# Performance work log

Measured on AMD Instinct MI355X. Metric: run time of the kernel, lower is better.

Reference implementation:

```python
import jax, jax.numpy as jnp
import numpy as np

N = 50000   # total nodes
E = 100000  # total edges
F = 64      # input node features
H = 128     # hidden_dim
HEADS = 4
B = 64      # number of graphs in the batch
S = 512     # num_stations
LC = 8      # num_line_colors


def setup_inputs() -> dict:
    key = jax.random.key(0)
    ks = jax.random.split(key, 40)
    w = lambda i, shape: (jax.random.normal(ks[i], shape, jnp.float32) * 0.02)
    inp = {
        'node_features': jax.random.normal(ks[0], (N, F), jnp.float32),
        'edge_index': jax.random.randint(ks[1], (2, E), 0, N),
        'batch': jnp.sort(jax.random.randint(ks[2], (N,), 0, B)),
        # initial projection F -> H
        'Wp': w(3, (F, H)), 'bp': w(4, (H,)),
        # TransformerConv 1: in H, out H, heads HEADS (concat)
        'Wq1': w(5, (H, HEADS * H)), 'bq1': w(6, (HEADS * H,)),
        'Wk1': w(7, (H, HEADS * H)), 'bk1': w(8, (HEADS * H,)),
        'Wv1': w(9, (H, HEADS * H)), 'bv1': w(10, (HEADS * H,)),
        'Ws1': w(11, (H, HEADS * H)), 'bs1': w(12, (HEADS * H,)),
        # TransformerConv 2: in HEADS*H, out H, heads 1
        'Wq2': w(13, (HEADS * H, H)), 'bq2': w(14, (H,)),
        'Wk2': w(15, (HEADS * H, H)), 'bk2': w(16, (H,)),
        'Wv2': w(17, (HEADS * H, H)), 'bv2': w(18, (H,)),
        'Ws2': w(19, (HEADS * H, H)), 'bs2': w(20, (H,)),
        # output heads
        'crW': w(21, (H, 1)),  'crb': w(22, (1,)),
        'hlW': w(23, (H, 4)),  'hlb': w(24, (4,)),
        'mtW': w(25, (H, 3)),  'mtb': w(26, (3,)),
        'p1W': w(27, (H, S)),  'p1b': w(28, (S,)),
        'p2W': w(29, (H, S)),  'p2b': w(30, (S,)),
        'dtW': w(31, (H, S)),  'dtb': w(32, (S,)),
        'slW': w(33, (H, LC)), 'slb': w(34, (LC,)),
    }
    return inp


def transformer_conv(x, src, dst, Wq, bq, Wk, bk, Wv, bv, Ws, bs, heads, out_ch):
    # PyG TransformerConv (beta=False, concat=True, root_weight=True):
    #   alpha_ij = softmax_j( (W_q x_i) . (W_k x_j) / sqrt(d) ) over in-edges of i
    #   out_i    = sum_j alpha_ij * (W_v x_j)  (concat heads) + W_skip x_i
    n = x.shape[0]
    q = (x @ Wq + bq).reshape(n, heads, out_ch)
    k = (x @ Wk + bk).reshape(n, heads, out_ch)
    v = (x @ Wv + bv).reshape(n, heads, out_ch)
    scores = jnp.sum(q[dst] * k[src], axis=-1) / jnp.sqrt(jnp.float32(out_ch))  # [E,heads]
    m = jax.ops.segment_max(scores, dst, num_segments=n)                        # per-target max
    e = jnp.exp(scores - m[dst])
    denom = jax.ops.segment_sum(e, dst, num_segments=n)
    alpha = e / (denom[dst] + 1e-16)                                            # [E,heads]
    out = jax.ops.segment_sum(alpha[:, :, None] * v[src], dst, num_segments=n)  # [N,heads,out]
    return out.reshape(n, heads * out_ch) + (x @ Ws + bs)


def reference(node_features, edge_index, batch, Wp, bp,
              Wq1, bq1, Wk1, bk1, Wv1, bv1, Ws1, bs1,
              Wq2, bq2, Wk2, bk2, Wv2, bv2, Ws2, bs2,
              crW, crb, hlW, hlb, mtW, mtb, p1W, p1b, p2W, p2b, dtW, dtb, slW, slb):
    src, dst = edge_index[0], edge_index[1]
    h = jax.nn.relu(node_features @ Wp + bp)
    h = jax.nn.relu(transformer_conv(h, src, dst, Wq1, bq1, Wk1, bk1, Wv1, bv1, Ws1, bs1, HEADS, H))
    h = jax.nn.relu(transformer_conv(h, src, dst, Wq2, bq2, Wk2, bk2, Wv2, bv2, Ws2, bs2, 1, H))
    # global mean pool over graphs
    counts = jax.ops.segment_sum(jnp.ones((h.shape[0],), h.dtype), batch, num_segments=B)
    g = jax.ops.segment_sum(h, batch, num_segments=B) / jnp.maximum(counts, 1.0)[:, None]  # [B,H]
    value = g @ crW + crb
    return (value,
            g @ hlW + hlb,
            g @ mtW + mtb,
            g @ p1W + p1b,
            g @ p2W + p2b,
            g @ dtW + dtb,
            g @ slW + slb)
```

## Files before the change

kernel.cpp:

```cpp
#include <hip/hip_runtime.h>
#include <hip/hip_bf16.h>

#define NN 50000
#define EE 100000
#define FF 64
#define HH 128
#define HEADS 4
#define BB 64
#define SS 512
#define LCC 8

__device__ __forceinline__ float b2f(ushort u) {
    return __uint_as_float(((unsigned)u) << 16);
}
__device__ __forceinline__ ushort f2b(float f) {
    unsigned u = __float_as_uint(f);
    unsigned r = (u + 0x7FFFu + ((u >> 16) & 1u)) >> 16;
    return (ushort)r;
}
__device__ __forceinline__ uint f2b_pk(float a, float b) {
    __hip_bfloat162 h = __float22bfloat162_rn(make_float2(a, b));
    return *reinterpret_cast<uint*>(&h);
}

__device__ __forceinline__ uint f2fp8x4(float a, float b, float c, float d) {
    int r = __builtin_amdgcn_cvt_pk_fp8_f32(a, b, 0, false);
    r = __builtin_amdgcn_cvt_pk_fp8_f32(c, d, r, true);
    return (uint)r;
}
__device__ __forceinline__ void fp8x4(uint u, float* f) {
    auto lo = __builtin_amdgcn_cvt_pk_f32_fp8((int)u, false);
    auto hi = __builtin_amdgcn_cvt_pk_f32_fp8((int)u, true);
    f[0] = lo[0]; f[1] = lo[1]; f[2] = hi[0]; f[3] = hi[1];
}

typedef __attribute__((ext_vector_type(4))) float f32x4;
typedef __attribute__((ext_vector_type(8))) short s16x8;
typedef __attribute__((ext_vector_type(4))) uint u32x4;

__device__ __forceinline__ void glls16(const ushort* g, ushort* l) {
    __builtin_amdgcn_global_load_lds((const __attribute__((address_space(1))) void*)g,
                                     (__attribute__((address_space(3))) void*)l, 16, 0, 0);
}

#define BM 128
#define BN 128
#define BK 64
#define EST 68

__global__ __launch_bounds__(256) void gemm_bf16(
    const ushort* __restrict__ A, const ushort* __restrict__ Bt,
    const float* __restrict__ bias,
    ushort* __restrict__ C1, int ld1,
    ushort* __restrict__ C2b, int mode,
    int M, int K, int relu, int gx, int gy)
{
    __shared__ __align__(16) ushort Sm[2 * BM * BK];
    ushort* As = Sm;
    ushort* Bs = Sm + BM * BK;

    const int bid  = blockIdx.x;
    const int xcd  = bid & 7;
    const int slot = bid >> 3;
    const int bx   = slot % gx;
    const int by   = xcd + 8 * (slot / gx);
    if (by >= gy) return;
    const int m0 = by * BM;
    const int n0 = bx * BN;

    const int t = threadIdx.x;
    const int lane = t & 63;
    const int wave = t >> 6;
    const int wm = (wave & 1) * 64;
    const int wn = (wave >> 1) * 64;
    const int lrow = lane & 15;
    const int g    = lane >> 4;

    const int wbase = n0 + wn;
    float bj[4];
#pragma unroll
    for (int j = 0; j < 4; ++j) bj[j] = bias[wbase + j * 16 + lrow];

    const int srow = (wave << 5) + (lane >> 3);
    const int scs  = lane & 7;

    const ushort* ga[4];
    const ushort* gb[4];
#pragma unroll
    for (int p = 0; p < 4; ++p) {
        const int row = srow + (p << 3);
        const int l   = scs ^ (row & 7);
        ga[p] = A + (size_t)min(m0 + row, M - 1) * K + (l << 3);
        gb[p] = Bt + (size_t)(n0 + row) * K + (l << 3);
    }
    const int ldsoff = (wave << 11);

    f32x4 acc[4][4];
#pragma unroll
    for (int i = 0; i < 4; ++i)
#pragma unroll
        for (int j = 0; j < 4; ++j)
            acc[i][j] = (f32x4){bj[j], bj[j], bj[j], bj[j]};

    for (int k0 = 0; k0 < K; k0 += BK) {
#pragma unroll
        for (int p = 0; p < 4; ++p) glls16(ga[p] + k0, As + ldsoff + (p << 9));
#pragma unroll
        for (int p = 0; p < 4; ++p) glls16(gb[p] + k0, Bs + ldsoff + (p << 9));
        __syncthreads();

#pragma unroll
        for (int kk = 0; kk < 2; ++kk) {
            s16x8 af[4], bf[4];
#pragma unroll
            for (int i = 0; i < 4; ++i) {
                const int R = wm + i * 16 + lrow;
                const int c = ((kk << 2) + g) ^ (R & 7);
                af[i] = *(const s16x8*)&As[(R << 6) + (c << 3)];
            }
#pragma unroll
            for (int j = 0; j < 4; ++j) {
                const int R = wn + j * 16 + lrow;
                const int c = ((kk << 2) + g) ^ (R & 7);
                bf[j] = *(const s16x8*)&Bs[(R << 6) + (c << 3)];
            }
#pragma unroll
            for (int i = 0; i < 4; ++i)
#pragma unroll
                for (int j = 0; j < 4; ++j)
                    acc[i][j] = __builtin_amdgcn_mfma_f32_16x16x32_bf16(af[i], bf[j], acc[i][j], 0, 0, 0);
        }
        __syncthreads();
    }

    float* Es = (float*)Sm + wave * (16 * EST);

    bool e8 = false;
    ushort* Cw = C1; int ldw = ld1; int cb = wbase;
    unsigned char* Cw8 = nullptr;
    if (mode == 1) {
        e8 = true;
        if (wbase < 512) {
            Cw8 = (unsigned char*)C1;
            ldw = 512;
        } else {
            const int u = wbase - 512;
            const int h = u >> 8;
            cb = u & 255;
            Cw8 = (unsigned char*)C2b + (size_t)h * NN * 256;
            ldw = 256;
        }
    } else if (mode == 2) {
        if (wbase < 128) { ldw = 128; }
        else {
            e8 = true;
            Cw8 = (unsigned char*)C2b;
            ldw = 384;
            cb = wbase - 128;
        }
    }

    const int rbase = (lane >> 4) * 4;
    const int rrow  = lane >> 2;
    const int rcol  = (lane & 3) << 4;

#pragma unroll
    for (int i = 0; i < 4; ++i) {
#pragma unroll
        for (int j = 0; j < 4; ++j)
#pragma unroll
            for (int r = 0; r < 4; ++r) {
                float v = acc[i][j][r];
                if (relu) v = fmaxf(v, 0.f);
                Es[(rbase + r) * EST + j * 16 + lrow] = v;
            }
        const int gm = m0 + wm + i * 16 + rrow;
        if (gm < M) {
            const float* srcp = Es + rrow * EST + rcol;
            f32x4 f0 = *(const f32x4*)(srcp + 0);
            f32x4 f1 = *(const f32x4*)(srcp + 4);
            f32x4 f2 = *(const f32x4*)(srcp + 8);
            f32x4 f3 = *(const f32x4*)(srcp + 12);
            if (!e8) {
                u32x4 o0, o1;
                o0[0] = f2b_pk(f0[0], f0[1]); o0[1] = f2b_pk(f0[2], f0[3]);
                o0[2] = f2b_pk(f1[0], f1[1]); o0[3] = f2b_pk(f1[2], f1[3]);
                o1[0] = f2b_pk(f2[0], f2[1]); o1[1] = f2b_pk(f2[2], f2[3]);
                o1[2] = f2b_pk(f3[0], f3[1]); o1[3] = f2b_pk(f3[2], f3[3]);
                ushort* dst = Cw + (size_t)gm * ldw + cb + rcol;
                *(u32x4*)(dst + 0) = o0;
                *(u32x4*)(dst + 8) = o1;
            } else {
                u32x4 o;
                o[0] = f2fp8x4(f0[0], f0[1], f0[2], f0[3]);
                o[1] = f2fp8x4(f1[0], f1[1], f1[2], f1[3]);
                o[2] = f2fp8x4(f2[0], f2[1], f2[2], f2[3]);
                o[3] = f2fp8x4(f3[0], f3[1], f3[2], f3[3]);
                *(u32x4*)(Cw8 + (size_t)gm * ldw + cb + rcol) = o;
            }
        }
    }
}

#define F1OFF  8192
#define F2OFF  204800
#define WTOTAL 466944
#define BTOT   2048
#define MWORK  (HEADS * 128 * 128 + HEADS * 128)

__global__ void prep_kernel(
    const float* __restrict__ Wp,
    const float* __restrict__ Wq1, const float* __restrict__ Wk1,
    const float* __restrict__ Wv1, const float* __restrict__ Ws1,
    const float* __restrict__ Wq2, const float* __restrict__ Wk2,
    const float* __restrict__ Wv2, const float* __restrict__ Ws2,
    const float* __restrict__ bs1, const float* __restrict__ bq1,
    const float* __restrict__ bv1, const float* __restrict__ bs2,
    const float* __restrict__ bq2, const float* __restrict__ bk2, const float* __restrict__ bv2,
    ushort* __restrict__ wt, float* __restrict__ bb)
{
    int t = blockIdx.x * 256 + threadIdx.x;
    if (t < WTOTAL) {
        float v;
        if (t < F1OFF) {
            int n = t >> 6, k = t & 63;
            v = Wp[k * 128 + n];
        } else if (t < F2OFF) {
            int u = t - F1OFF;
            int n = u >> 7, k = u & 127;
            if (n < 512) v = Ws1[k * 512 + n] * 16.0f;
            else {
                int r = n - 512;
                int h = r >> 8, c = r & 255;
                if (c < 128) return;
                v = Wv1[k * 512 + h * 128 + (c - 128)] * 16.0f;
            }
        } else {
            int u = t - F2OFF;
            int n = u >> 9, k = u & 511;
            if (n < 128) v = Ws2[k * 128 + n];
            else {
                int r = n - 128;
                const float* W = (r < 128) ? Wq2 : (r < 256) ? Wk2 : Wv2;
                v = W[k * 128 + (r & 127)] * 16.0f;
            }
        }
        wt[t] = f2b(v);
    } else if (t < WTOTAL + BTOT) {
        int u = t - WTOTAL;
        float v;
        if (u < 512) v = bs1[u] * 16.0f;
        else if (u < 1536) {
            int r = u - 512;
            int h = r >> 8, c = r & 255;
            if (c < 128) return;
            v = bv1[h * 128 + (c - 128)] * 16.0f;
        } else {
            int c = u - 1536;
            v = (c < 128) ? bs2[c]
              : (c < 256) ? bq2[c - 128] * 16.0f
              : (c < 384) ? bk2[c - 256] * 16.0f : bv2[c - 384] * 16.0f;
        }
        bb[u] = v;
    } else if (t < WTOTAL + BTOT + MWORK) {
        int m = t - (WTOTAL + BTOT);
        if (m < HEADS * 128 * 128) {
            int h = m >> 14;
            int rem = m & 16383;
            int b = rem >> 7, a = rem & 127;
            const float* wq = Wq1 + a * 512 + h * 128;
            const float* wk = Wk1 + b * 512 + h * 128;
            float acc = 0.f;
#pragma unroll 8
            for (int d = 0; d < 128; ++d) acc += wq[d] * wk[d];
            wt[F1OFF + (size_t)(512 + h * 256 + b) * 128 + a] = f2b(acc * 16.0f);
        } else {
            int u = m - HEADS * 128 * 128;
            int h = u >> 7, b = u & 127;
            const float* wk = Wk1 + b * 512 + h * 128;
            const float* bq = bq1 + h * 128;
            float acc = 0.f;
#pragma unroll 8
            for (int d = 0; d < 128; ++d) acc += wk[d] * bq[d];
            bb[512 + h * 256 + b] = acc * 16.0f;
        }
    }
}

__global__ void cvt_fill_kernel(const float4* __restrict__ in, uint2* __restrict__ out, int n4,
                                unsigned* __restrict__ fillp, int filln)
{
    int i = blockIdx.x * 256 + threadIdx.x;
    if (i < n4) {
        float4 v = in[i];
        uint2 o;
        o.x = f2b_pk(v.x, v.y);
        o.y = f2b_pk(v.z, v.w);
        out[i] = o;
    } else {
        int j = i - n4;
        if (j < filln) fillp[j] = 0u;
    }
}

__global__ void hist_kernel(const int* __restrict__ dst, int* __restrict__ cnt, int E) {
    int e = blockIdx.x * 256 + threadIdx.x;
    if (e < E) atomicAdd(&cnt[dst[e]], 1);
}

#define SCAN_B 1024
__global__ void scan_bsum_kernel(const int* __restrict__ cnt, int* __restrict__ bsum, int n) {
    __shared__ int sd[256];
    int tid = threadIdx.x;
    int base = blockIdx.x * SCAN_B + tid * 4;
    int s = 0;
#pragma unroll
    for (int j = 0; j < 4; ++j) if (base + j < n) s += cnt[base + j];
    sd[tid] = s;
    __syncthreads();
    for (int off = 128; off > 0; off >>= 1) {
        if (tid < off) sd[tid] += sd[tid + off];
        __syncthreads();
    }
    if (tid == 0) bsum[blockIdx.x] = sd[0];
}

__global__ void scan_final_kernel(const int* __restrict__ cnt, const int* __restrict__ bsum,
                                  int* __restrict__ rowptr, int* __restrict__ cursor, int n) {
    __shared__ int sd[256];
    __shared__ int sb[256];
    int tid = threadIdx.x;
    sb[tid] = (tid < blockIdx.x) ? bsum[tid] : 0;
    __syncthreads();
    for (int off = 128; off > 0; off >>= 1) {
        if (tid < off) sb[tid] += sb[tid + off];
        __syncthreads();
    }
    const int bbase = sb[0];

    int base = blockIdx.x * SCAN_B + tid * 4;
    int v[4]; int s = 0;
#pragma unroll
    for (int j = 0; j < 4; ++j) { v[j] = (base + j < n) ? cnt[base + j] : 0; s += v[j]; }
    sd[tid] = s;
    __syncthreads();
    for (int off = 1; off < 256; off <<= 1) {
        int t2 = (tid >= off) ? sd[tid - off] : 0;
        __syncthreads();
        sd[tid] += t2;
        __syncthreads();
    }
    int acc = bbase + sd[tid] - s;
#pragma unroll
    for (int j = 0; j < 4; ++j) {
        if (base + j < n) cursor[base + j] = acc;
        acc += v[j];
        if (base + j < n) rowptr[base + j + 1] = acc;
    }
    if (blockIdx.x == 0 && tid == 0) rowptr[0] = 0;
}

__global__ void bucket_kernel(const int* __restrict__ src, const int* __restrict__ dst,
                              int* __restrict__ cursor, int* __restrict__ srcs, int E) {
    int e = blockIdx.x * 256 + threadIdx.x;
    if (e >= E) return;
    int p = atomicAdd(&cursor[dst[e]], 1);
    srcs[p] = src[e];
}

__global__ __launch_bounds__(256) void gather4_kernel(
    const unsigned char* __restrict__ Qb, const ushort* __restrict__ Kb,
    const int* __restrict__ rowptr, const int* __restrict__ srcs,
    const unsigned char* __restrict__ s8,
    ushort* __restrict__ outp, float scale, int n)
{
    int i = blockIdx.x * 4 + (threadIdx.x >> 6);
    int lane = threadIdx.x & 63;
    if (i >= n) return;
    const int h = lane >> 4;
    const int l = lane & 15;

    const unsigned char* Qh = Qb + (size_t)h * ((size_t)NN * 256);

    uint2 uq = *(const uint2*)(Qh + (size_t)i * 256 + l * 8);
    float q[8];
    fp8x4(uq.x, q); fp8x4(uq.y, q + 4);

    int p0 = rowptr[i], p1 = rowptr[i + 1];
    float den = 0.f;
    float o[8] = {0.f, 0.f, 0.f, 0.f, 0.f, 0.f, 0.f, 0.f};
    int p = p0;
    for (; p + 2 <= p1; p += 2) {
        int s0 = srcs[p], s1 = srcs[p + 1];
        s16x8 ka = *(const s16x8*)(Kb + (size_t)s0 * 128 + l * 8);
        s16x8 kb = *(const s16x8*)(Kb + (size_t)s1 * 128 + l * 8);
        uint2 va = *(const uint2*)(Qh + (size_t)s0 * 256 + 128 + l * 8);
        uint2 vb = *(const uint2*)(Qh + (size_t)s1 * 256 + 128 + l * 8);
        float da = 0.f, db = 0.f;
#pragma unroll
        for (int d = 0; d < 8; ++d) {
            da += q[d] * b2f((ushort)ka[d]);
            db += q[d] * b2f((ushort)kb[d]);
        }
#pragma unroll
        for (int off = 8; off > 0; off >>= 1) {
            da += __shfl_xor(da, off, 64);
            db += __shfl_xor(db, off, 64);
        }
        float ea = __expf(da * scale);
        float eb = __expf(db * scale);
        den += ea + eb;
        float fa[8], fb[8];
        fp8x4(va.x, fa); fp8x4(va.y, fa + 4);
        fp8x4(vb.x, fb); fp8x4(vb.y, fb + 4);
#pragma unroll
        for (int d = 0; d < 8; ++d) o[d] += ea * fa[d] + eb * fb[d];
    }
    if (p < p1) {
        int s = srcs[p];
        s16x8 kv = *(const s16x8*)(Kb + (size_t)s * 128 + l * 8);
        uint2 vv = *(const uint2*)(Qh + (size_t)s * 256 + 128 + l * 8);
        float d0 = 0.f;
#pragma unroll
        for (int d = 0; d < 8; ++d) d0 += q[d] * b2f((ushort)kv[d]);
#pragma unroll
        for (int off = 8; off > 0; off >>= 1) d0 += __shfl_xor(d0, off, 64);
        float e = __expf(d0 * scale);
        den += e;
        float fv[8];
        fp8x4(vv.x, fv); fp8x4(vv.y, fv + 4);
#pragma unroll
        for (int d = 0; d < 8; ++d) o[d] += e * fv[d];
    }
    float invd = 1.0f / (den + 1e-16f);
    uint2 sk = *(const uint2*)(s8 + (size_t)i * 512 + h * 128 + l * 8);
    float skf[8];
    fp8x4(sk.x, skf); fp8x4(sk.y, skf + 4);
    float r[8];
#pragma unroll
    for (int d = 0; d < 8; ++d) r[d] = 0.0625f * fmaxf(skf[d] + o[d] * invd, 0.f);
    u32x4 ov;
    ov[0] = f2b_pk(r[0], r[1]);
    ov[1] = f2b_pk(r[2], r[3]);
    ov[2] = f2b_pk(r[4], r[5]);
    ov[3] = f2b_pk(r[6], r[7]);
    *(u32x4*)(outp + (size_t)i * 512 + h * 128 + l * 8) = ov;
}

__global__ __launch_bounds__(256) void edge_gather_kernel(
    const unsigned char* __restrict__ qkv,
    const int* __restrict__ rowptr, const int* __restrict__ srcs,
    const ushort* __restrict__ skip,
    ushort* __restrict__ outp, float scale, int n)
{
    int i = blockIdx.x * 4 + (threadIdx.x >> 6);
    int lane = threadIdx.x & 63;
    if (i >= n) return;
    const int g = lane >> 4;
    const int l = lane & 15;

    uint2 uq = *(const uint2*)(qkv + (size_t)i * 384 + l * 8);
    float q[8];
    fp8x4(uq.x, q); fp8x4(uq.y, q + 4);

    int p0 = rowptr[i], p1 = rowptr[i + 1];
    float den = 0.f;
    float o[8] = {0.f, 0.f, 0.f, 0.f, 0.f, 0.f, 0.f, 0.f};
    for (int pb = p0; pb < p1; pb += 4) {
        int p = pb + g;
        bool act = p < p1;
        int s = srcs[act ? p : p0];
        const unsigned char* row = qkv + (size_t)s * 384;
        uint2 kv = *(const uint2*)(row + 128 + l * 8);
        uint2 vv = *(const uint2*)(row + 256 + l * 8);
        float kf[8];
        fp8x4(kv.x, kf); fp8x4(kv.y, kf + 4);
        float d0 = 0.f;
#pragma unroll
        for (int d = 0; d < 8; ++d) d0 += q[d] * kf[d];
#pragma unroll
        for (int off = 8; off > 0; off >>= 1) d0 += __shfl_xor(d0, off, 64);
        float e = act ? __expf(d0 * scale) : 0.f;
        den += e;
        float vf[8];
        fp8x4(vv.x, vf); fp8x4(vv.y, vf + 4);
#pragma unroll
        for (int d = 0; d < 8; ++d) o[d] += e * vf[d];
    }
#pragma unroll
    for (int off = 16; off < 64; off <<= 1) {
        den += __shfl_xor(den, off, 64);
#pragma unroll
        for (int d = 0; d < 8; ++d) o[d] += __shfl_xor(o[d], off, 64);
    }
    if (g == 0) {
        float inv = 0.0625f / (den + 1e-16f);
        s16x8 sk = *(const s16x8*)(skip + (size_t)i * 128 + l * 8);
        float r[8];
#pragma unroll
        for (int d = 0; d < 8; ++d) r[d] = b2f((ushort)sk[d]) + o[d] * inv;
        u32x4 ov;
        ov[0] = f2b_pk(r[0], r[1]);
        ov[1] = f2b_pk(r[2], r[3]);
        ov[2] = f2b_pk(r[4], r[5]);
        ov[3] = f2b_pk(r[6], r[7]);
        *(u32x4*)(outp + (size_t)i * 128 + l * 8) = ov;
    }
}

__global__ __launch_bounds__(256) void pool_kernel(
    const ushort* __restrict__ h, const int* __restrict__ batch,
    float* __restrict__ gsum, float* __restrict__ cnt, int n)
{
    int wave = threadIdx.x >> 6, lane = threadIdx.x & 63;
    int start = blockIdx.x * 256 + wave * 64;
    int end = min(start + 64, n);
    if (start >= end) return;
    int cur = batch[start];
    float a0 = 0.f, a1 = 0.f;
    int run = 0;
    for (int node = start; node < end; ++node) {
        int g = batch[node];
        if (g != cur) {
            atomicAdd(&gsum[cur * HH + 2 * lane], a0);
            atomicAdd(&gsum[cur * HH + 2 * lane + 1], a1);
            if (lane == 0) atomicAdd(&cnt[cur], (float)run);
            cur = g; a0 = a1 = 0.f; run = 0;
        }
        uint x = ((const uint*)h)[(size_t)node * 64 + lane];
        a0 += fmaxf(b2f((ushort)x), 0.f);
        a1 += fmaxf(b2f((ushort)(x >> 16)), 0.f);
        ++run;
    }
    atomicAdd(&gsum[cur * HH + 2 * lane], a0);
    atomicAdd(&gsum[cur * HH + 2 * lane + 1], a1);
    if (lane == 0) atomicAdd(&cnt[cur], (float)run);
}

__global__ void pool_fin_kernel(const float* __restrict__ gsum,
                                const float* __restrict__ cnt, float* __restrict__ g)
{
    int i = blockIdx.x * blockDim.x + threadIdx.x;
    if (i < BB * HH) g[i] = gsum[i] / fmaxf(cnt[i / HH], 1.0f);
}

__global__ void out_heads_kernel(
    const float* __restrict__ g,
    const float* __restrict__ w0, const float* __restrict__ b0,
    const float* __restrict__ w1, const float* __restrict__ b1,
    const float* __restrict__ w2, const float* __restrict__ b2,
    const float* __restrict__ w3, const float* __restrict__ b3,
    const float* __restrict__ w4, const float* __restrict__ b4,
    const float* __restrict__ w5, const float* __restrict__ b5,
    const float* __restrict__ w6, const float* __restrict__ b6,
    float* __restrict__ out, int total)
{
    int t = blockIdx.x * blockDim.x + threadIdx.x;
    if (t >= total) return;
    const float* W; const float* bias; int cols; int local;
    if      (t < 64)    { W = w0; bias = b0; cols = 1;   local = t; }
    else if (t < 320)   { W = w1; bias = b1; cols = 4;   local = t - 64; }
    else if (t < 512)   { W = w2; bias = b2; cols = 3;   local = t - 320; }
    else if (t < 33280) { W = w3; bias = b3; cols = SS;  local = t - 512; }
    else if (t < 66048) { W = w4; bias = b4; cols = SS;  local = t - 33280; }
    else if (t < 98816) { W = w5; bias = b5; cols = SS;  local = t - 66048; }
    else                { W = w6; bias = b6; cols = LCC; local = t - 98816; }
    int b = local / cols, c = local % cols;
    const float* gr = g + b * HH;
    float acc = bias[c];
#pragma unroll 8
    for (int i = 0; i < HH; ++i) acc += gr[i] * W[i * cols + c];
    out[t] = acc;
}

extern "C" void kernel_launch(void* const* d_in, const int* in_sizes, int n_in,
                              void* d_out, int out_size, void* d_ws, size_t ws_size,
                              hipStream_t stream)
{
    (void)in_sizes; (void)n_in; (void)out_size; (void)ws_size;

    const float* nf   = (const float*)d_in[0];
    const int*   ei   = (const int*)d_in[1];
    const int*   src  = ei;
    const int*   dst  = ei + EE;
    const int*   batch= (const int*)d_in[2];
    const float* Wp   = (const float*)d_in[3];
    const float* bp   = (const float*)d_in[4];
    const float* Wq1  = (const float*)d_in[5];
    const float* bq1  = (const float*)d_in[6];
    const float* Wk1  = (const float*)d_in[7];
    const float* bk1  = (const float*)d_in[8];
    const float* Wv1  = (const float*)d_in[9];
    const float* bv1  = (const float*)d_in[10];
    const float* Ws1  = (const float*)d_in[11];
    const float* bs1  = (const float*)d_in[12];
    const float* Wq2  = (const float*)d_in[13];
    const float* bq2  = (const float*)d_in[14];
    const float* Wk2  = (const float*)d_in[15];
    const float* bk2  = (const float*)d_in[16];
    const float* Wv2  = (const float*)d_in[17];
    const float* bv2  = (const float*)d_in[18];
    const float* Ws2  = (const float*)d_in[19];
    const float* bs2  = (const float*)d_in[20];
    const float* crW  = (const float*)d_in[21];
    const float* crb  = (const float*)d_in[22];
    const float* hlW  = (const float*)d_in[23];
    const float* hlb  = (const float*)d_in[24];
    const float* mtW  = (const float*)d_in[25];
    const float* mtb  = (const float*)d_in[26];
    const float* p1W  = (const float*)d_in[27];
    const float* p1b  = (const float*)d_in[28];
    const float* p2W  = (const float*)d_in[29];
    const float* p2b  = (const float*)d_in[30];
    const float* dtW  = (const float*)d_in[31];
    const float* dtb  = (const float*)d_in[32];
    const float* slW  = (const float*)d_in[33];
    const float* slb  = (const float*)d_in[34];
    float* out = (float*)d_out;

    (void)bk1;

    unsigned char* base = (unsigned char*)d_ws;
    unsigned char* Qb8  = base;
    ushort* nfb  = (ushort*)base;
    ushort* h2sb = (ushort*)base;
    unsigned char* qkv8 = base + (size_t)NN * 256;
    ushort* h2   = (ushort*)(base + (size_t)NN * 640);
    ushort* h0b  = (ushort*)(base + (size_t)NN * 1024);
    ushort* h1b  = (ushort*)(base + (size_t)NN * 1280);
    unsigned char* s8 = base + (size_t)NN * 2304;
    ushort* wt   = (ushort*)(base + (size_t)NN * 2816);
    float*  bb   = (float*)(wt + WTOTAL);
    int*    rowptr = (int*)(bb + BTOT);
    int*    srcs   = rowptr + NN + 1;
    int*    cnt    = srcs + EE;
    float*  gsum   = (float*)(cnt + NN);
    float*  cntb   = gsum + BB * HH;
    int*    cursor = (int*)(cntb + BB);
    int*    bsum   = cursor + NN;
    float*  gbuf   = (float*)(bsum + 64);

    const float scale = 0.08838834764831845f;
    const dim3 blk(256);
    const int gy  = (NN + BM - 1) / BM;
    const int gyp = ((gy + 7) / 8) * 8;
    const int nb = (NN + SCAN_B - 1) / SCAN_B;

    prep_kernel<<<(WTOTAL + BTOT + MWORK + 255) / 256, blk, 0, stream>>>(
        Wp, Wq1, Wk1, Wv1, Ws1, Wq2, Wk2, Wv2, Ws2,
        bs1, bq1, bv1, bs2, bq2, bk2, bv2, wt, bb);

    const int n4 = NN * FF / 4;
    const int filln = NN + BB * HH + BB;
    cvt_fill_kernel<<<(n4 + filln + 255) / 256, blk, 0, stream>>>(
        (const float4*)nf, (uint2*)nfb, n4, (unsigned*)cnt, filln);

    hist_kernel<<<(EE + 255) / 256, blk, 0, stream>>>(dst, cnt, EE);
    scan_bsum_kernel<<<nb, blk, 0, stream>>>(cnt, bsum, NN);
    scan_final_kernel<<<nb, blk, 0, stream>>>(cnt, bsum, rowptr, cursor, NN);
    bucket_kernel<<<(EE + 255) / 256, blk, 0, stream>>>(src, dst, cursor, srcs, EE);

    gemm_bf16<<<dim3(1 * gyp), blk, 0, stream>>>(
        nfb, wt, bp, h0b, HH, h0b, 0, NN, FF, 1, 1, gy);

    gemm_bf16<<<dim3(12 * gyp), blk, 0, stream>>>(
        h0b, wt + F1OFF, bb, (ushort*)s8, 512, (ushort*)Qb8, 1, NN, HH, 0, 12, gy);

    gather4_kernel<<<(NN + 3) / 4, blk, 0, stream>>>(
        Qb8, h0b, rowptr, srcs, s8, h1b, scale * 0.0625f, NN);

    gemm_bf16<<<dim3(4 * gyp), blk, 0, stream>>>(
        h1b, wt + F2OFF, bb + 1536, h2sb, 128, (ushort*)qkv8, 2, NN, 4 * HH, 0, 4, gy);

    edge_gather_kernel<<<(NN + 3) / 4, blk, 0, stream>>>(
        qkv8, rowptr, srcs, h2sb, h2, scale * 0.00390625f, NN);

    pool_kernel<<<(NN + 255) / 256, blk, 0, stream>>>(h2, batch, gsum, cntb, NN);
    pool_fin_kernel<<<(BB * HH + 255) / 256, blk, 0, stream>>>(gsum, cntb, gbuf);

    const int total = BB * (1 + 4 + 3 + SS + SS + SS + LCC);
    out_heads_kernel<<<(total + 255) / 256, blk, 0, stream>>>(
        gbuf, crW, crb, hlW, hlb, mtW, mtb, p1W, p1b, p2W, p2b, dtW, dtb, slW, slb, out, total);
}
```

Before: 330.5 us.

## Fuse input projection into first QKV GEMM and merge prep/cvt/pool-finalize kernels

A new fused kernel computes the F->H projection with ReLU directly into LDS for each 128-row tile, then immediately runs the layer-1 Q/K/V/skip GEMM from that LDS tile. This removes the separate projection GEMM launch and the h0 round trip through global memory. The cost is that every column block recomputes the small projection, and only bx==0 writes h0b. The bf16 conversion and zero fill are folded into prep_kernel, and pool finalization is folded into out_heads. The skip load in gather4 is also hoisted earlier to overlap its latency.

```diff
diff --git a/kernel.cpp b/kernel.cpp
--- a/kernel.cpp
+++ b/kernel.cpp
@@ -47,6 +47,194 @@
 #define BN 128
 #define BK 64
 #define EST 68
+
+__global__ __launch_bounds__(256) void f1_fused(
+    const ushort* __restrict__ nfb, const ushort* __restrict__ wpt,
+    const float* __restrict__ bp,
+    const ushort* __restrict__ Bt, const float* __restrict__ bias,
+    unsigned char* __restrict__ s8, unsigned char* __restrict__ Qb8,
+    ushort* __restrict__ h0b, int M, int gx, int gy)
+{
+    __shared__ __align__(16) ushort Sm[16384 + 8192 + 512];
+    ushort* As2 = Sm;
+    ushort* Bs  = Sm + 16384;
+    float*  Es  = (float*)(Sm + 16384);
+
+    const int bid  = blockIdx.x;
+    const int xcd  = bid & 7;
+    const int slot = bid >> 3;
+    const int bx   = slot % gx;
+    const int by   = xcd + 8 * (slot / gx);
+    if (by >= gy) return;
+    const int m0 = by * BM;
+    const int n0 = bx * BN;
+
+    const int t = threadIdx.x;
+    const int lane = t & 63;
+    const int wave = t >> 6;
+    const int wm = (wave & 1) * 64;
+    const int wn = (wave >> 1) * 64;
+    const int lrow = lane & 15;
+    const int g    = lane >> 4;
+
+    const int rbase = (lane >> 4) * 4;
+    const int rrow  = lane >> 2;
+    const int rcol  = (lane & 3) << 4;
+
+    float* Ew = Es + wave * (16 * EST);
+
+    f32x4 acc[4][4];
+
+    {
+        float bpj[4];
+#pragma unroll
+        for (int j = 0; j < 4; ++j) bpj[j] = bp[wn + j * 16 + lrow];
+#pragma unroll
+        for (int i = 0; i < 4; ++i)
+#pragma unroll
+            for (int j = 0; j < 4; ++j)
+                acc[i][j] = (f32x4){bpj[j], bpj[j], bpj[j], bpj[j]};
+
+        s16x8 afp[4][2], bfp[4][2];
+#pragma unroll
+        for (int i = 0; i < 4; ++i) {
+            const size_t ar = (size_t)min(m0 + wm + i * 16 + lrow, M - 1) * 64;
+#pragma unroll
+            for (int kk = 0; kk < 2; ++kk)
+                afp[i][kk] = *(const s16x8*)&nfb[ar + ((kk << 2) + g) * 8];
+        }
+#pragma unroll
+        for (int j = 0; j < 4; ++j) {
+            const size_t br = (size_t)(wn + j * 16 + lrow) * 64;
+#pragma unroll
+            for (int kk = 0; kk < 2; ++kk)
+                bfp[j][kk] = *(const s16x8*)&wpt[br + ((kk << 2) + g) * 8];
+        }
+#pragma unroll
+        for (int kk = 0; kk < 2; ++kk)
+#pragma unroll
+            for (int i = 0; i < 4; ++i)
+#pragma unroll
+                for (int j = 0; j < 4; ++j)
+                    acc[i][j] = __builtin_amdgcn_mfma_f32_16x16x32_bf16(afp[i][kk], bfp[j][kk], acc[i][j], 0, 0, 0);
+
+#pragma unroll
+        for (int i = 0; i < 4; ++i) {
+#pragma unroll
+            for (int j = 0; j < 4; ++j)
+#pragma unroll
+                for (int r = 0; r < 4; ++r)
+                    Ew[(rbase + r) * EST + j * 16 + lrow] = fmaxf(acc[i][j][r], 0.f);
+            const float* srcp = Ew + rrow * EST + rcol;
+            f32x4 f0 = *(const f32x4*)(srcp + 0);
+            f32x4 f1 = *(const f32x4*)(srcp + 4);
+            f32x4 f2 = *(const f32x4*)(srcp + 8);
+            f32x4 f3 = *(const f32x4*)(srcp + 12);
+            u32x4 o0, o1;
+            o0[0] = f2b_pk(f0[0], f0[1]); o0[1] = f2b_pk(f0[2], f0[3]);
+            o0[2] = f2b_pk(f1[0], f1[1]); o0[3] = f2b_pk(f1[2], f1[3]);
+            o1[0] = f2b_pk(f2[0], f2[1]); o1[1] = f2b_pk(f2[2], f2[3]);
+            o1[2] = f2b_pk(f3[0], f3[1]); o1[3] = f2b_pk(f3[2], f3[3]);
+            const int R = wm + i * 16 + rrow;
+            const int G0 = (wn + rcol) >> 3;
+            *(u32x4*)&As2[(R << 7) + ((G0 ^ (R & 7)) << 3)]       = o0;
+            *(u32x4*)&As2[(R << 7) + (((G0 + 1) ^ (R & 7)) << 3)] = o1;
+            if (bx == 0) {
+                const int gm = m0 + R;
+                if (gm < M) {
+                    ushort* dst = h0b + (size_t)gm * 128 + wn + rcol;
+                    *(u32x4*)(dst + 0) = o0;
+                    *(u32x4*)(dst + 8) = o1;
+                }
+            }
+        }
+    }
+    __syncthreads();
+
+    const int wbase = n0 + wn;
+    {
+        float bj[4];
+#pragma unroll
+        for (int j = 0; j < 4; ++j) bj[j] = bias[wbase + j * 16 + lrow];
+#pragma unroll
+        for (int i = 0; i < 4; ++i)
+#pragma unroll
+            for (int j = 0; j < 4; ++j)
+                acc[i][j] = (f32x4){bj[j], bj[j], bj[j], bj[j]};
+    }
+
+    const int srow = (wave << 5) + (lane >> 3);
+    const int scs  = lane & 7;
+    const ushort* gb[4];
+#pragma unroll
+    for (int p = 0; p < 4; ++p) {
+        const int row = srow + (p << 3);
+        const int l   = scs ^ (row & 7);
+        gb[p] = Bt + (size_t)(n0 + row) * 128 + (l << 3);
+    }
+    const int ldsoff = (wave << 11);
+
+    for (int k0 = 0; k0 < 128; k0 += BK) {
+#pragma unroll
+        for (int p = 0; p < 4; ++p) glls16(gb[p] + k0, Bs + ldsoff + (p << 9));
+        __syncthreads();
+#pragma unroll
+        for (int kk = 0; kk < 2; ++kk) {
+            s16x8 af[4], bf[4];
+#pragma unroll
+            for (int i = 0; i < 4; ++i) {
+                const int R = wm + i * 16 + lrow;
+                const int G = (k0 >> 3) + (kk << 2) + g;
+                af[i] = *(const s16x8*)&As2[(R << 7) + ((G ^ (R & 7)) << 3)];
+            }
+#pragma unroll
+            for (int j = 0; j < 4; ++j) {
+                const int R = wn + j * 16 + lrow;
+                const int c = ((kk << 2) + g) ^ (R & 7);
+                bf[j] = *(const s16x8*)&Bs[(R << 6) + (c << 3)];
+            }
+#pragma unroll
+            for (int i = 0; i < 4; ++i)
+#pragma unroll
+                for (int j = 0; j < 4; ++j)
+                    acc[i][j] = __builtin_amdgcn_mfma_f32_16x16x32_bf16(af[i], bf[j], acc[i][j], 0, 0, 0);
+        }
+        __syncthreads();
+    }
+
+    unsigned char* Cw8; int ldw, cb;
+    if (wbase < 512) { Cw8 = s8; ldw = 512; cb = wbase; }
+    else {
+        const int u = wbase - 512;
+        const int h = u >> 8;
+        cb = u & 255;
+        Cw8 = Qb8 + (size_t)h * NN * 256;
+        ldw = 256;
+    }
+
+#pragma unroll
+    for (int i = 0; i < 4; ++i) {
+#pragma unroll
+        for (int j = 0; j < 4; ++j)
+#pragma unroll
+            for (int r = 0; r < 4; ++r)
+                Ew[(rbase + r) * EST + j * 16 + lrow] = acc[i][j][r];
+        const int gm = m0 + wm + i * 16 + rrow;
+        if (gm < M) {
+            const float* srcp = Ew + rrow * EST + rcol;
+            f32x4 f0 = *(const f32x4*)(srcp + 0);
+            f32x4 f1 = *(const f32x4*)(srcp + 4);
+            f32x4 f2 = *(const f32x4*)(srcp + 8);
+            f32x4 f3 = *(const f32x4*)(srcp + 12);
+            u32x4 o;
+            o[0] = f2fp8x4(f0[0], f0[1], f0[2], f0[3]);
+            o[1] = f2fp8x4(f1[0], f1[1], f1[2], f1[3]);
+            o[2] = f2fp8x4(f2[0], f2[1], f2[2], f2[3]);
+            o[3] = f2fp8x4(f3[0], f3[1], f3[2], f3[3]);
+            *(u32x4*)(Cw8 + (size_t)gm * ldw + cb + rcol) = o;
+        }
+    }
+}
 
 __global__ __launch_bounds__(256) void gemm_bf16(
     const ushort* __restrict__ A, const ushort* __restrict__ Bt,
@@ -138,19 +326,7 @@
     bool e8 = false;
     ushort* Cw = C1; int ldw = ld1; int cb = wbase;
     unsigned char* Cw8 = nullptr;
-    if (mode == 1) {
-        e8 = true;
-        if (wbase < 512) {
-            Cw8 = (unsigned char*)C1;
-            ldw = 512;
-        } else {
-            const int u = wbase - 512;
-            const int h = u >> 8;
-            cb = u & 255;
-            Cw8 = (unsigned char*)C2b + (size_t)h * NN * 256;
-            ldw = 256;
-        }
-    } else if (mode == 2) {
+    if (mode == 2) {
         if (wbase < 128) { ldw = 128; }
         else {
             e8 = true;
@@ -207,8 +383,10 @@
 #define WTOTAL 466944
 #define BTOT   2048
 #define MWORK  (HEADS * 128 * 128 + HEADS * 128)
+#define CVTN   (NN * FF / 4)
 
 __global__ void prep_kernel(
+    const float* __restrict__ nf, ushort* __restrict__ nfb,
     const float* __restrict__ Wp,
     const float* __restrict__ Wq1, const float* __restrict__ Wk1,
     const float* __restrict__ Wv1, const float* __restrict__ Ws1,
@@ -217,9 +395,19 @@
     const float* __restrict__ bs1, const float* __restrict__ bq1,
     const float* __restrict__ bv1, const float* __restrict__ bs2,
     const float* __restrict__ bq2, const float* __restrict__ bk2, const float* __restrict__ bv2,
-    ushort* __restrict__ wt, float* __restrict__ bb)
+    ushort* __restrict__ wt, float* __restrict__ bb,
+    unsigned* __restrict__ zerop, int zn)
 {
-    int t = blockIdx.x * 256 + threadIdx.x;
+    int t0 = blockIdx.x * 256 + threadIdx.x;
+    if (t0 < CVTN) {
+        float4 v = ((const float4*)nf)[t0];
+        uint2 o;
+        o.x = f2b_pk(v.x, v.y);
+        o.y = f2b_pk(v.z, v.w);
+        ((uint2*)nfb)[t0] = o;
+        return;
+    }
+    int t = t0 - CVTN;
     if (t < WTOTAL) {
         float v;
         if (t < F1OFF) {
@@ -284,22 +472,9 @@
             for (int d = 0; d < 128; ++d) acc += wk[d] * bq[d];
             bb[512 + h * 256 + b] = acc * 16.0f;
         }
-    }
-}
-
-__global__ void cvt_fill_kernel(const float4* __restrict__ in, uint2* __restrict__ out, int n4,
-                                unsigned* __restrict__ fillp, int filln)
-{
-    int i = blockIdx.x * 256 + threadIdx.x;
-    if (i < n4) {
-        float4 v = in[i];
-        uint2 o;
-        o.x = f2b_pk(v.x, v.y);
-        o.y = f2b_pk(v.z, v.w);
-        out[i] = o;
     } else {
-        int j = i - n4;
-        if (j < filln) fillp[j] = 0u;
+        int z = t - (WTOTAL + BTOT + MWORK);
+        if (z < zn) zerop[z] = 0u;
     }
 }
 
@@ -383,6 +558,7 @@
     const unsigned char* Qh = Qb + (size_t)h * ((size_t)NN * 256);
 
     uint2 uq = *(const uint2*)(Qh + (size_t)i * 256 + l * 8);
+    uint2 sk = *(const uint2*)(s8 + (size_t)i * 512 + h * 128 + l * 8);
     float q[8];
     fp8x4(uq.x, q); fp8x4(uq.y, q + 4);
 
@@ -433,7 +609,6 @@
         for (int d = 0; d < 8; ++d) o[d] += e * fv[d];
     }
     float invd = 1.0f / (den + 1e-16f);
-    uint2 sk = *(const uint2*)(s8 + (size_t)i * 512 + h * 128 + l * 8);
     float skf[8];
     fp8x4(sk.x, skf); fp8x4(sk.y, skf + 4);
     float r[8];
@@ -537,15 +712,8 @@
     if (lane == 0) atomicAdd(&cnt[cur], (float)run);
 }
 
-__global__ void pool_fin_kernel(const float* __restrict__ gsum,
-                                const float* __restrict__ cnt, float* __restrict__ g)
-{
-    int i = blockIdx.x * blockDim.x + threadIdx.x;
-    if (i < BB * HH) g[i] = gsum[i] / fmaxf(cnt[i / HH], 1.0f);
-}
-
 __global__ void out_heads_kernel(
-    const float* __restrict__ g,
+    const float* __restrict__ gsum, const float* __restrict__ cntb,
     const float* __restrict__ w0, const float* __restrict__ b0,
     const float* __restrict__ w1, const float* __restrict__ b1,
     const float* __restrict__ w2, const float* __restrict__ b2,
@@ -566,11 +734,12 @@
     else if (t < 98816) { W = w5; bias = b5; cols = SS;  local = t - 66048; }
     else                { W = w6; bias = b6; cols = LCC; local = t - 98816; }
     int b = local / cols, c = local % cols;
-    const float* gr = g + b * HH;
-    float acc = bias[c];
+    const float* gr = gsum + b * HH;
+    float inv = 1.0f / fmaxf(cntb[b], 1.0f);
+    float s = 0.f;
 #pragma unroll 8
-    for (int i = 0; i < HH; ++i) acc += gr[i] * W[i * cols + c];
-    out[t] = acc;
+    for (int i = 0; i < HH; ++i) s += gr[i] * W[i * cols + c];
+    out[t] = bias[c] + s * inv;
 }
 
 extern "C" void kernel_launch(void* const* d_in, const int* in_sizes, int n_in,
@@ -622,7 +791,6 @@
 
     unsigned char* base = (unsigned char*)d_ws;
     unsigned char* Qb8  = base;
-    ushort* nfb  = (ushort*)base;
     ushort* h2sb = (ushort*)base;
     unsigned char* qkv8 = base + (size_t)NN * 256;
     ushort* h2   = (ushort*)(base + (size_t)NN * 640);
@@ -638,7 +806,7 @@
     float*  cntb   = gsum + BB * HH;
     int*    cursor = (int*)(cntb + BB);
     int*    bsum   = cursor + NN;
-    float*  gbuf   = (float*)(bsum + 64);
+    ushort* nfb  = (ushort*)(base + (size_t)NN * 2944);
 
     const float scale = 0.08838834764831845f;
     const dim3 blk(256);
@@ -646,25 +814,19 @@
     const int gyp = ((gy + 7) / 8) * 8;
     const int nb = (NN + SCAN_B - 1) / SCAN_B;
 
-    prep_kernel<<<(WTOTAL + BTOT + MWORK + 255) / 256, blk, 0, stream>>>(
-        Wp, Wq1, Wk1, Wv1, Ws1, Wq2, Wk2, Wv2, Ws2,
-        bs1, bq1, bv1, bs2, bq2, bk2, bv2, wt, bb);
-
-    const int n4 = NN * FF / 4;
     const int filln = NN + BB * HH + BB;
-    cvt_fill_kernel<<<(n4 + filln + 255) / 256, blk, 0, stream>>>(
-        (const float4*)nf, (uint2*)nfb, n4, (unsigned*)cnt, filln);
+    const int ptot = CVTN + WTOTAL + BTOT + MWORK + filln;
+    prep_kernel<<<(ptot + 255) / 256, blk, 0, stream>>>(
+        nf, nfb, Wp, Wq1, Wk1, Wv1, Ws1, Wq2, Wk2, Wv2, Ws2,
+        bs1, bq1, bv1, bs2, bq2, bk2, bv2, wt, bb, (unsigned*)cnt, filln);
 
     hist_kernel<<<(EE + 255) / 256, blk, 0, stream>>>(dst, cnt, EE);
     scan_bsum_kernel<<<nb, blk, 0, stream>>>(cnt, bsum, NN);
     scan_final_kernel<<<nb, blk, 0, stream>>>(cnt, bsum, rowptr, cursor, NN);
     bucket_kernel<<<(EE + 255) / 256, blk, 0, stream>>>(src, dst, cursor, srcs, EE);
 
-    gemm_bf16<<<dim3(1 * gyp), blk, 0, stream>>>(
-        nfb, wt, bp, h0b, HH, h0b, 0, NN, FF, 1, 1, gy);
-
-    gemm_bf16<<<dim3(12 * gyp), blk, 0, stream>>>(
-        h0b, wt + F1OFF, bb, (ushort*)s8, 512, (ushort*)Qb8, 1, NN, HH, 0, 12, gy);
+    f1_fused<<<dim3(12 * gyp), blk, 0, stream>>>(
+        nfb, wt, bp, wt + F1OFF, bb, s8, Qb8, h0b, NN, 12, gy);
 
     gather4_kernel<<<(NN + 3) / 4, blk, 0, stream>>>(
         Qb8, h0b, rowptr, srcs, s8, h1b, scale * 0.0625f, NN);
@@ -676,9 +838,8 @@
         qkv8, rowptr, srcs, h2sb, h2, scale * 0.00390625f, NN);
 
     pool_kernel<<<(NN + 255) / 256, blk, 0, stream>>>(h2, batch, gsum, cntb, NN);
-    pool_fin_kernel<<<(BB * HH + 255) / 256, blk, 0, stream>>>(gsum, cntb, gbuf);
 
     const int total = BB * (1 + 4 + 3 + SS + SS + SS + LCC);
     out_heads_kernel<<<(total + 255) / 256, blk, 0, stream>>>(
-        gbuf, crW, crb, hlW, hlb, mtW, mtb, p1W, p1b, p2W, p2b, dtW, dtb, slW, slb, out, total);
-}
+        gsum, cntb, crW, crb, hlW, hlb, mtW, mtb, p1W, p1b, p2W, p2b, dtW, dtb, slW, slb, out, total);
+}
```

Measured after the change: 359.2 us. +8.7%, slower.

## Pack per-source K and V into fp8 rows and fuse small prep kernels

Applied to the files above, without the earlier changes.

The first GEMM now also writes h0 as fp8, scaled by 16, into a 640-byte per-node row. The second GEMM places the V heads in the same row, so gather4 fetches K and V for each source node from one contiguous fp8 row instead of a bf16 K plus a separate per-head V plane. Q moves to a per-node 512-byte layout, and the skip load is hoisted. Input conversion and zero-fill merge into prep_kernel, and the pool-finish kernel folds into the output heads, cutting launches. The cost is fp8 precision on K in layer one plus extra epilogue writes.

```diff
diff --git a/kernel.cpp b/kernel.cpp
--- a/kernel.cpp
+++ b/kernel.cpp
@@ -52,8 +52,8 @@
     const ushort* __restrict__ A, const ushort* __restrict__ Bt,
     const float* __restrict__ bias,
     ushort* __restrict__ C1, int ld1,
-    ushort* __restrict__ C2b, int mode,
-    int M, int K, int relu, int gx, int gy)
+    unsigned char* __restrict__ C2b, unsigned char* __restrict__ C3,
+    int mode, int M, int K, int relu, int gx, int gy)
 {
     __shared__ __align__(16) ushort Sm[2 * BM * BK];
     ushort* As = Sm;
@@ -135,29 +135,24 @@
 
     float* Es = (float*)Sm + wave * (16 * EST);
 
-    bool e8 = false;
+    int dsel = 0;
     ushort* Cw = C1; int ldw = ld1; int cb = wbase;
-    unsigned char* Cw8 = nullptr;
-    if (mode == 1) {
-        e8 = true;
-        if (wbase < 512) {
-            Cw8 = (unsigned char*)C1;
-            ldw = 512;
-        } else {
+    unsigned char* Cw8 = nullptr; int ldw8 = 0, cb8 = 0;
+    if (mode == 0) {
+        dsel = 2; Cw8 = C2b; ldw8 = 640; cb8 = wbase;
+    } else if (mode == 1) {
+        dsel = 1;
+        if (wbase < 512) { Cw8 = (unsigned char*)C1; ldw8 = 512; cb8 = wbase; }
+        else {
             const int u = wbase - 512;
             const int h = u >> 8;
-            cb = u & 255;
-            Cw8 = (unsigned char*)C2b + (size_t)h * NN * 256;
-            ldw = 256;
-        }
-    } else if (mode == 2) {
-        if (wbase < 128) { ldw = 128; }
-        else {
-            e8 = true;
-            Cw8 = (unsigned char*)C2b;
-            ldw = 384;
-            cb = wbase - 128;
-        }
+            const int c = u & 255;
+            if (c < 128) { Cw8 = C2b; ldw8 = 512; cb8 = h * 128 + c; }
+            else         { Cw8 = C3;  ldw8 = 640; cb8 = 128 + h * 128 + (c - 128); }
+        }
+    } else {
+        if (wbase < 128) { dsel = 0; ldw = 128; }
+        else { dsel = 1; Cw8 = C2b; ldw8 = 384; cb8 = wbase - 128; }
     }
 
     const int rbase = (lane >> 4) * 4;
@@ -181,7 +176,7 @@
             f32x4 f1 = *(const f32x4*)(srcp + 4);
             f32x4 f2 = *(const f32x4*)(srcp + 8);
             f32x4 f3 = *(const f32x4*)(srcp + 12);
-            if (!e8) {
+            if (dsel != 1) {
                 u32x4 o0, o1;
                 o0[0] = f2b_pk(f0[0], f0[1]); o0[1] = f2b_pk(f0[2], f0[3]);
                 o0[2] = f2b_pk(f1[0], f1[1]); o0[3] = f2b_pk(f1[2], f1[3]);
@@ -190,13 +185,15 @@
                 ushort* dst = Cw + (size_t)gm * ldw + cb + rcol;
                 *(u32x4*)(dst + 0) = o0;
                 *(u32x4*)(dst + 8) = o1;
-            } else {
+            }
+            if (dsel >= 1) {
+                const float ms = (dsel == 2) ? 16.0f : 1.0f;
                 u32x4 o;
-                o[0] = f2fp8x4(f0[0], f0[1], f0[2], f0[3]);
-                o[1] = f2fp8x4(f1[0], f1[1], f1[2], f1[3]);
-                o[2] = f2fp8x4(f2[0], f2[1], f2[2], f2[3]);
-                o[3] = f2fp8x4(f3[0], f3[1], f3[2], f3[3]);
-                *(u32x4*)(Cw8 + (size_t)gm * ldw + cb + rcol) = o;
+                o[0] = f2fp8x4(ms * f0[0], ms * f0[1], ms * f0[2], ms * f0[3]);
+                o[1] = f2fp8x4(ms * f1[0], ms * f1[1], ms * f1[2], ms * f1[3]);
+                o[2] = f2fp8x4(ms * f2[0], ms * f2[1], ms * f2[2], ms * f2[3]);
+                o[3] = f2fp8x4(ms * f3[0], ms * f3[1], ms * f3[2], ms * f3[3]);
+                *(u32x4*)(Cw8 + (size_t)gm * ldw8 + cb8 + rcol) = o;
             }
         }
     }
@@ -207,8 +204,10 @@
 #define WTOTAL 466944
 #define BTOT   2048
 #define MWORK  (HEADS * 128 * 128 + HEADS * 128)
+#define CVTN   (NN * FF / 4)
 
 __global__ void prep_kernel(
+    const float* __restrict__ nf, ushort* __restrict__ nfb,
     const float* __restrict__ Wp,
     const float* __restrict__ Wq1, const float* __restrict__ Wk1,
     const float* __restrict__ Wv1, const float* __restrict__ Ws1,
@@ -217,9 +216,19 @@
     const float* __restrict__ bs1, const float* __restrict__ bq1,
     const float* __restrict__ bv1, const float* __restrict__ bs2,
     const float* __restrict__ bq2, const float* __restrict__ bk2, const float* __restrict__ bv2,
-    ushort* __restrict__ wt, float* __restrict__ bb)
+    ushort* __restrict__ wt, float* __restrict__ bb,
+    unsigned* __restrict__ zerop, int zn)
 {
-    int t = blockIdx.x * 256 + threadIdx.x;
+    int t0 = blockIdx.x * 256 + threadIdx.x;
+    if (t0 < CVTN) {
+        float4 v = ((const float4*)nf)[t0];
+        uint2 o;
+        o.x = f2b_pk(v.x, v.y);
+        o.y = f2b_pk(v.z, v.w);
+        ((uint2*)nfb)[t0] = o;
+        return;
+    }
+    int t = t0 - CVTN;
     if (t < WTOTAL) {
         float v;
         if (t < F1OFF) {
@@ -284,22 +293,9 @@
             for (int d = 0; d < 128; ++d) acc += wk[d] * bq[d];
             bb[512 + h * 256 + b] = acc * 16.0f;
         }
-    }
-}
-
-__global__ void cvt_fill_kernel(const float4* __restrict__ in, uint2* __restrict__ out, int n4,
-                                unsigned* __restrict__ fillp, int filln)
-{
-    int i = blockIdx.x * 256 + threadIdx.x;
-    if (i < n4) {
-        float4 v = in[i];
-        uint2 o;
-        o.x = f2b_pk(v.x, v.y);
-        o.y = f2b_pk(v.z, v.w);
-        out[i] = o;
     } else {
-        int j = i - n4;
-        if (j < filln) fillp[j] = 0u;
+        int z = t - (WTOTAL + BTOT + MWORK);
+        if (z < zn) zerop[z] = 0u;
     }
 }
 
@@ -369,7 +365,7 @@
 }
 
 __global__ __launch_bounds__(256) void gather4_kernel(
-    const unsigned char* __restrict__ Qb, const ushort* __restrict__ Kb,
+    const unsigned char* __restrict__ Qu, const unsigned char* __restrict__ eD,
     const int* __restrict__ rowptr, const int* __restrict__ srcs,
     const unsigned char* __restrict__ s8,
     ushort* __restrict__ outp, float scale, int n)
@@ -379,10 +375,10 @@
     if (i >= n) return;
     const int h = lane >> 4;
     const int l = lane & 15;
-
-    const unsigned char* Qh = Qb + (size_t)h * ((size_t)NN * 256);
-
-    uint2 uq = *(const uint2*)(Qh + (size_t)i * 256 + l * 8);
+    const int vo = 128 + h * 128 + l * 8;
+
+    uint2 uq = *(const uint2*)(Qu + (size_t)i * 512 + h * 128 + l * 8);
+    uint2 sk = *(const uint2*)(s8 + (size_t)i * 512 + h * 128 + l * 8);
     float q[8];
     fp8x4(uq.x, q); fp8x4(uq.y, q + 4);
 
@@ -392,15 +388,20 @@
     int p = p0;
     for (; p + 2 <= p1; p += 2) {
         int s0 = srcs[p], s1 = srcs[p + 1];
-        s16x8 ka = *(const s16x8*)(Kb + (size_t)s0 * 128 + l * 8);
-        s16x8 kb = *(const s16x8*)(Kb + (size_t)s1 * 128 + l * 8);
-        uint2 va = *(const uint2*)(Qh + (size_t)s0 * 256 + 128 + l * 8);
-        uint2 vb = *(const uint2*)(Qh + (size_t)s1 * 256 + 128 + l * 8);
+        const unsigned char* ra = eD + (size_t)s0 * 640;
+        const unsigned char* rb = eD + (size_t)s1 * 640;
+        uint2 ka = *(const uint2*)(ra + l * 8);
+        uint2 kb = *(const uint2*)(rb + l * 8);
+        uint2 va = *(const uint2*)(ra + vo);
+        uint2 vb = *(const uint2*)(rb + vo);
+        float kaf[8], kbf[8];
+        fp8x4(ka.x, kaf); fp8x4(ka.y, kaf + 4);
+        fp8x4(kb.x, kbf); fp8x4(kb.y, kbf + 4);
         float da = 0.f, db = 0.f;
 #pragma unroll
         for (int d = 0; d < 8; ++d) {
-            da += q[d] * b2f((ushort)ka[d]);
-            db += q[d] * b2f((ushort)kb[d]);
+            da += q[d] * kaf[d];
+            db += q[d] * kbf[d];
         }
 #pragma unroll
         for (int off = 8; off > 0; off >>= 1) {
@@ -418,11 +419,14 @@
     }
     if (p < p1) {
         int s = srcs[p];
-        s16x8 kv = *(const s16x8*)(Kb + (size_t)s * 128 + l * 8);
-        uint2 vv = *(const uint2*)(Qh + (size_t)s * 256 + 128 + l * 8);
+        const unsigned char* row = eD + (size_t)s * 640;
+        uint2 kv = *(const uint2*)(row + l * 8);
+        uint2 vv = *(const uint2*)(row + vo);
+        float kf[8];
+        fp8x4(kv.x, kf); fp8x4(kv.y, kf + 4);
         float d0 = 0.f;
 #pragma unroll
-        for (int d = 0; d < 8; ++d) d0 += q[d] * b2f((ushort)kv[d]);
+        for (int d = 0; d < 8; ++d) d0 += q[d] * kf[d];
 #pragma unroll
         for (int off = 8; off > 0; off >>= 1) d0 += __shfl_xor(d0, off, 64);
         float e = __expf(d0 * scale);
@@ -433,7 +437,6 @@
         for (int d = 0; d < 8; ++d) o[d] += e * fv[d];
     }
     float invd = 1.0f / (den + 1e-16f);
-    uint2 sk = *(const uint2*)(s8 + (size_t)i * 512 + h * 128 + l * 8);
     float skf[8];
     fp8x4(sk.x, skf); fp8x4(sk.y, skf + 4);
     float r[8];
@@ -537,15 +540,8 @@
     if (lane == 0) atomicAdd(&cnt[cur], (float)run);
 }
 
-__global__ void pool_fin_kernel(const float* __restrict__ gsum,
-                                const float* __restrict__ cnt, float* __restrict__ g)
-{
-    int i = blockIdx.x * blockDim.x + threadIdx.x;
-    if (i < BB * HH) g[i] = gsum[i] / fmaxf(cnt[i / HH], 1.0f);
-}
-
 __global__ void out_heads_kernel(
-    const float* __restrict__ g,
+    const float* __restrict__ gsum, const float* __restrict__ cntb,
     const float* __restrict__ w0, const float* __restrict__ b0,
     const float* __restrict__ w1, const float* __restrict__ b1,
     const float* __restrict__ w2, const float* __restrict__ b2,
@@ -566,11 +562,12 @@
     else if (t < 98816) { W = w5; bias = b5; cols = SS;  local = t - 66048; }
     else                { W = w6; bias = b6; cols = LCC; local = t - 98816; }
     int b = local / cols, c = local % cols;
-    const float* gr = g + b * HH;
-    float acc = bias[c];
+    const float* gr = gsum + b * HH;
+    float inv = 1.0f / fmaxf(cntb[b], 1.0f);
+    float s = 0.f;
 #pragma unroll 8
-    for (int i = 0; i < HH; ++i) acc += gr[i] * W[i * cols + c];
-    out[t] = acc;
+    for (int i = 0; i < HH; ++i) s += gr[i] * W[i * cols + c];
+    out[t] = bias[c] + s * inv;
 }
 
 extern "C" void kernel_launch(void* const* d_in, const int* in_sizes, int n_in,
@@ -621,15 +618,16 @@
     (void)bk1;
 
     unsigned char* base = (unsigned char*)d_ws;
-    unsigned char* Qb8  = base;
-    ushort* nfb  = (ushort*)base;
+    unsigned char* edgeD = base;
+    unsigned char* Qu8   = base + (size_t)NN * 640;
     ushort* h2sb = (ushort*)base;
     unsigned char* qkv8 = base + (size_t)NN * 256;
     ushort* h2   = (ushort*)(base + (size_t)NN * 640);
-    ushort* h0b  = (ushort*)(base + (size_t)NN * 1024);
-    ushort* h1b  = (ushort*)(base + (size_t)NN * 1280);
-    unsigned char* s8 = base + (size_t)NN * 2304;
-    ushort* wt   = (ushort*)(base + (size_t)NN * 2816);
+    unsigned char* s8 = base + (size_t)NN * 1152;
+    ushort* h0b  = (ushort*)(base + (size_t)NN * 1664);
+    ushort* h1b  = (ushort*)(base + (size_t)NN * 1920);
+    ushort* nfb  = h1b;
+    ushort* wt   = (ushort*)(base + (size_t)NN * 2944);
     float*  bb   = (float*)(wt + WTOTAL);
     int*    rowptr = (int*)(bb + BTOT);
     int*    srcs   = rowptr + NN + 1;
@@ -638,7 +636,6 @@
     float*  cntb   = gsum + BB * HH;
     int*    cursor = (int*)(cntb + BB);
     int*    bsum   = cursor + NN;
-    float*  gbuf   = (float*)(bsum + 64);
 
     const float scale = 0.08838834764831845f;
     const dim3 blk(256);
@@ -646,14 +643,11 @@
     const int gyp = ((gy + 7) / 8) * 8;
     const int nb = (NN + SCAN_B - 1) / SCAN_B;
 
-    prep_kernel<<<(WTOTAL + BTOT + MWORK + 255) / 256, blk, 0, stream>>>(
-        Wp, Wq1, Wk1, Wv1, Ws1, Wq2, Wk2, Wv2, Ws2,
-        bs1, bq1, bv1, bs2, bq2, bk2, bv2, wt, bb);
-
-    const int n4 = NN * FF / 4;
     const int filln = NN + BB * HH + BB;
-    cvt_fill_kernel<<<(n4 + filln + 255) / 256, blk, 0, stream>>>(
-        (const float4*)nf, (uint2*)nfb, n4, (unsigned*)cnt, filln);
+    const int ptot = CVTN + WTOTAL + BTOT + MWORK + filln;
+    prep_kernel<<<(ptot + 255) / 256, blk, 0, stream>>>(
+        nf, nfb, Wp, Wq1, Wk1, Wv1, Ws1, Wq2, Wk2, Wv2, Ws2,
+        bs1, bq1, bv1, bs2, bq2, bk2, bv2, wt, bb, (unsigned*)cnt, filln);
 
     hist_kernel<<<(EE + 255) / 256, blk, 0, stream>>>(dst, cnt, EE);
     scan_bsum_kernel<<<nb, blk, 0, stream>>>(cnt, bsum, NN);
@@ -661,24 +655,23 @@
     bucket_kernel<<<(EE + 255) / 256, blk, 0, stream>>>(src, dst, cursor, srcs, EE);
 
     gemm_bf16<<<dim3(1 * gyp), blk, 0, stream>>>(
-        nfb, wt, bp, h0b, HH, h0b, 0, NN, FF, 1, 1, gy);
+        nfb, wt, bp, h0b, HH, edgeD, nullptr, 0, NN, FF, 1, 1, gy);
 
     gemm_bf16<<<dim3(12 * gyp), blk, 0, stream>>>(
-        h0b, wt + F1OFF, bb, (ushort*)s8, 512, (ushort*)Qb8, 1, NN, HH, 0, 12, gy);
+        h0b, wt + F1OFF, bb, (ushort*)s8, 512, Qu8, edgeD, 1, NN, HH, 0, 12, gy);
 
     gather4_kernel<<<(NN + 3) / 4, blk, 0, stream>>>(
-        Qb8, h0b, rowptr, srcs, s8, h1b, scale * 0.0625f, NN);
+        Qu8, edgeD, rowptr, srcs, s8, h1b, scale * 0.00390625f, NN);
 
     gemm_bf16<<<dim3(4 * gyp), blk, 0, stream>>>(
-        h1b, wt + F2OFF, bb + 1536, h2sb, 128, (ushort*)qkv8, 2, NN, 4 * HH, 0, 4, gy);
+        h1b, wt + F2OFF, bb + 1536, h2sb, 128, qkv8, nullptr, 2, NN, 4 * HH, 0, 4, gy);
 
     edge_gather_kernel<<<(NN + 3) / 4, blk, 0, stream>>>(
         qkv8, rowptr, srcs, h2sb, h2, scale * 0.00390625f, NN);
 
     pool_kernel<<<(NN + 255) / 256, blk, 0, stream>>>(h2, batch, gsum, cntb, NN);
-    pool_fin_kernel<<<(BB * HH + 255) / 256, blk, 0, stream>>>(gsum, cntb, gbuf);
 
     const int total = BB * (1 + 4 + 3 + SS + SS + SS + LCC);
     out_heads_kernel<<<(total + 255) / 256, blk, 0, stream>>>(
-        gbuf, crW, crb, hlW, hlb, mtW, mtb, p1W, p1b, p2W, p2b, dtW, dtb, slW, slb, out, total);
-}
+        gsum, cntb, crW, crb, hlW, hlb, mtW, mtb, p1W, p1b, p2W, p2b, dtW, dtb, slW, slb, out, total);
+}
```

Measured after the change: 341.7 us. 1.03x slower.
